# Kernel tuning notes

Measured on AMD Instinct MI355X. Metric: run time of the kernel, lower is better.

Reference implementation:

```python
import jax, jax.numpy as jnp
import numpy as np

N = 100000
E = 1600000
IN_DIM, HID, Z = 128, 64, 32


def gcn_conv(x, src, dst, num_nodes, W, b):
    """PyG GCNConv: add self-loops, symmetric deg^-1/2 normalization.
    x: [N, F_in]; src/dst: [E] int (self-loops already appended by caller wrapper).
    """
    h = x @ W  # [N, F_out] transform first (PyG order)
    ones = jnp.ones(src.shape[0], dtype=x.dtype)
    deg = jax.ops.segment_sum(ones, dst, num_segments=num_nodes)  # in-degree incl. self-loop
    dinv = jnp.where(deg > 0, jax.lax.rsqrt(deg), 0.0)
    norm = dinv[src] * dinv[dst]  # [E]
    msgs = h[src] * norm[:, None]  # [E, F_out] irregular gather
    out = jax.ops.segment_sum(msgs, dst, num_segments=num_nodes)  # scatter-add
    return out + b


def setup_inputs() -> dict:
    key = jax.random.key(0)
    ks = jax.random.split(key, 10)
    x = jax.random.normal(ks[0], (N, IN_DIM), dtype=jnp.float32)
    edge_index = jax.random.randint(ks[1], (2, E), 0, N, dtype=jnp.int64)

    def glorot(k, fan_in, fan_out):
        s = jnp.sqrt(6.0 / (fan_in + fan_out))
        return jax.random.uniform(k, (fan_in, fan_out), jnp.float32, -s, s)

    return {
        "x": x,
        "edge_index": edge_index,
        "W1": glorot(ks[2], IN_DIM, HID),
        "b1": jnp.zeros((HID,), jnp.float32),
        "W2": glorot(ks[3], HID, Z),
        "b2": jnp.zeros((Z,), jnp.float32),
        "Wmu": glorot(ks[4], Z, Z),
        "bmu": jnp.zeros((Z,), jnp.float32),
        "Wlv": glorot(ks[5], Z, Z),
        "blv": jnp.zeros((Z,), jnp.float32),
    }


def reference(x, edge_index, W1, b1, W2, b2, Wmu, bmu, Wlv, blv):
    num_nodes = x.shape[0]
    loop = jnp.arange(num_nodes, dtype=edge_index.dtype)
    src = jnp.concatenate([edge_index[0], loop])  # self-loops appended
    dst = jnp.concatenate([edge_index[1], loop])
    h = jax.nn.relu(gcn_conv(x, src, dst, num_nodes, W1, b1))
    h = gcn_conv(h, src, dst, num_nodes, W2, b2)
    mu = h @ Wmu + bmu
    logvar = h @ Wlv + blv
    return (mu, logvar)
```

## Files before the change

kernel.cpp:

```cpp
#include <hip/hip_runtime.h>

#define N_NODES 100000
#define N_EDGES 1600000
#define IN_F   128
#define HID_F  64
#define Z_F    32
#define NBUK   782
#define BCAP   3072
#define P1T    4096
#define P1_BLOCKS ((N_EDGES + P1T - 1) / P1T)
#define AGG_CAP 2048

typedef unsigned int uint32;
typedef __attribute__((ext_vector_type(8))) short bf16x8;
typedef __attribute__((ext_vector_type(4))) float f32x4;

__device__ __forceinline__ unsigned short f2bf(float f) {
    unsigned u = __float_as_uint(f);
    u = (u + 0x7FFF + ((u >> 16) & 1)) >> 16;
    return (unsigned short)u;
}
__device__ __forceinline__ uint32 pack2bf(float lo, float hi) {
    return (uint32)f2bf(lo) | ((uint32)f2bf(hi) << 16);
}
__device__ __forceinline__ float bflo(uint32 u) { return __uint_as_float(u << 16); }
__device__ __forceinline__ float bfhi(uint32 u) { return __uint_as_float(u & 0xFFFF0000u); }

__global__ __launch_bounds__(256) void phase1_kernel(const int* __restrict__ ei,
                                                     int* __restrict__ gcur,
                                                     uint32* __restrict__ pairs) {
    __shared__ int hist[NBUK];
    __shared__ int lbase[NBUK];
    __shared__ int gbase[NBUK];
    __shared__ int lcur[NBUK];
    __shared__ uint32 stage[P1T];
    __shared__ unsigned short sbid[P1T];
    __shared__ int part[256];
    int tid = threadIdx.x;
    int e0 = blockIdx.x * P1T;
    int ecnt = N_EDGES - e0; if (ecnt > P1T) ecnt = P1T;
    for (int b = tid; b < NBUK; b += 256) { hist[b] = 0; lcur[b] = 0; }
    __syncthreads();
    for (int k = tid; k < ecnt; k += 256)
        atomicAdd(&hist[ei[N_EDGES + e0 + k] >> 7], 1);
    __syncthreads();
    int t4 = tid * 4;
    int l0 = 0, l1 = 0, l2 = 0, l3 = 0, s = 0;
    if (t4 + 0 < NBUK) { l0 = hist[t4 + 0]; s += l0; }
    if (t4 + 1 < NBUK) { l1 = hist[t4 + 1]; s += l1; }
    if (t4 + 2 < NBUK) { l2 = hist[t4 + 2]; s += l2; }
    if (t4 + 3 < NBUK) { l3 = hist[t4 + 3]; s += l3; }
    part[tid] = s;
    __syncthreads();
    for (int off = 1; off < 256; off <<= 1) {
        int add = (tid >= off) ? part[tid - off] : 0;
        __syncthreads();
        part[tid] += add;
        __syncthreads();
    }
    int run = part[tid] - s;
    if (t4 + 0 < NBUK) { lbase[t4 + 0] = run; run += l0; }
    if (t4 + 1 < NBUK) { lbase[t4 + 1] = run; run += l1; }
    if (t4 + 2 < NBUK) { lbase[t4 + 2] = run; run += l2; }
    if (t4 + 3 < NBUK) { lbase[t4 + 3] = run; run += l3; }
    for (int b = tid; b < NBUK; b += 256) {
        int h = hist[b];
        gbase[b] = h ? atomicAdd(&gcur[b], h) : 0;
    }
    __syncthreads();
    for (int k = tid; k < ecnt; k += 256) {
        int sN = ei[e0 + k];
        int d  = ei[N_EDGES + e0 + k];
        int b = d >> 7;
        int slot = lbase[b] + atomicAdd(&lcur[b], 1);
        stage[slot] = (uint32)sN | ((uint32)(d & 127) << 17);
        sbid[slot] = (unsigned short)b;
    }
    __syncthreads();
    for (int k = tid; k < ecnt; k += 256) {
        int b = sbid[k];
        int r = gbase[b] + (k - lbase[b]);
        if (r < BCAP) pairs[(size_t)b * BCAP + r] = stage[k];
    }
}

__global__ void prep_kernel(const int* __restrict__ gcur,
                            const float* __restrict__ W1, const float* __restrict__ W2,
                            const float* __restrict__ Wmu, const float* __restrict__ Wlv,
                            int* __restrict__ bucketBase, int* __restrict__ rowptr,
                            unsigned short* __restrict__ Wt1,
                            unsigned short* __restrict__ Wt2,
                            unsigned short* __restrict__ Wth) {
    __shared__ int s[1024];
    int t = threadIdx.x;
    int v = (t < NBUK) ? gcur[t] : 0;
    s[t] = v;
    __syncthreads();
    for (int off = 1; off < 1024; off <<= 1) {
        int add = (t >= off) ? s[t - off] : 0;
        __syncthreads();
        s[t] += add;
        __syncthreads();
    }
    if (t < NBUK) bucketBase[t] = s[t] - v;
    if (t == 0) rowptr[N_NODES] = N_EDGES;
    for (int i = t; i < IN_F * HID_F; i += 1024) {
        int n = i >> 7, k = i & 127;
        Wt1[i] = f2bf(W1[k * HID_F + n]);
    }
    for (int i = t; i < HID_F * Z_F; i += 1024) {
        int n = i >> 6, k = i & 63;
        Wt2[i] = f2bf(W2[k * Z_F + n]);
    }
    for (int i = t; i < Z_F * 64; i += 1024) {
        int n = i >> 5, k = i & 31;
        Wth[i] = f2bf(n < 32 ? Wmu[k * Z_F + n] : Wlv[k * Z_F + (n - 32)]);
    }
}

__global__ __launch_bounds__(256) void phase2_kernel(const uint32* __restrict__ pairs,
                                                     const int* __restrict__ gcur,
                                                     const int* __restrict__ bucketBase,
                                                     int* __restrict__ rowptr,
                                                     float* __restrict__ dinv,
                                                     int* __restrict__ col) {
    __shared__ int lhist[128];
    __shared__ int lscan[128];
    __shared__ int lcur[128];
    __shared__ int stage[BCAP];
    int b = blockIdx.x;
    int tid = threadIdx.x;
    int cnt_b = gcur[b];
    if (cnt_b > BCAP) cnt_b = BCAP;
    int gbase = bucketBase[b];
    int node0 = b << 7;
    int nb = N_NODES - node0;
    if (nb > 128) nb = 128;
    if (tid < 128) { lhist[tid] = 0; lcur[tid] = 0; }
    __syncthreads();
    const uint32* pb = pairs + (size_t)b * BCAP;
    for (int k = tid; k < cnt_b; k += 256) atomicAdd(&lhist[pb[k] >> 17], 1);
    __syncthreads();
    int v = (tid < 128) ? lhist[tid] : 0;
    if (tid < 128) lscan[tid] = v;
    __syncthreads();
    for (int off = 1; off < 128; off <<= 1) {
        int add = (tid < 128 && tid >= off) ? lscan[tid - off] : 0;
        __syncthreads();
        if (tid < 128) lscan[tid] += add;
        __syncthreads();
    }
    if (tid < 128) lscan[tid] -= v;
    __syncthreads();
    if (tid < nb) {
        rowptr[node0 + tid] = gbase + lscan[tid];
        dinv[node0 + tid] = rsqrtf((float)(lhist[tid] + 1));
    }
    for (int k = tid; k < cnt_b; k += 256) {
        uint32 u = pb[k];
        int ld = u >> 17;
        int r = atomicAdd(&lcur[ld], 1);
        stage[lscan[ld] + r] = (int)(u & 0x1FFFF);
    }
    __syncthreads();
    for (int k = tid; k < cnt_b; k += 256) col[gbase + k] = stage[k];
}

__global__ __launch_bounds__(256) void gemm1_kernel(const float* __restrict__ x,
                                                    const unsigned short* __restrict__ Wt1,
                                                    const float* __restrict__ dinv,
                                                    unsigned short* __restrict__ t1) {
    __shared__ unsigned short Cs[64 * 72];
    __shared__ float dv[64];
    int tid = threadIdx.x;
    int node0 = blockIdx.x * 64;
    if (tid < 64) {
        int n = node0 + tid;
        dv[tid] = (n < N_NODES) ? dinv[n] : 0.f;
    }
    __syncthreads();
    int w = tid >> 6, lane = tid & 63;
    int m = lane & 15, quad = lane >> 4;
    int row = w * 16 + m;
    int node = node0 + row;
    const float* xr = x + (size_t)min(node, N_NODES - 1) * IN_F;
    f32x4 acc0 = {0.f, 0.f, 0.f, 0.f};
    f32x4 acc1 = acc0, acc2 = acc0, acc3 = acc0;
#pragma unroll
    for (int ks = 0; ks < 4; ks++) {
        int kb = ks * 32 + quad * 8;
        float4 f0 = *(const float4*)(xr + kb);
        float4 f1 = *(const float4*)(xr + kb + 4);
        union { bf16x8 v; unsigned short u[8]; } A;
        A.u[0] = f2bf(f0.x); A.u[1] = f2bf(f0.y); A.u[2] = f2bf(f0.z); A.u[3] = f2bf(f0.w);
        A.u[4] = f2bf(f1.x); A.u[5] = f2bf(f1.y); A.u[6] = f2bf(f1.z); A.u[7] = f2bf(f1.w);
        bf16x8 b0 = *(const bf16x8*)&Wt1[(0 * 16 + m) * IN_F + kb];
        bf16x8 b1 = *(const bf16x8*)&Wt1[(1 * 16 + m) * IN_F + kb];
        bf16x8 b2 = *(const bf16x8*)&Wt1[(2 * 16 + m) * IN_F + kb];
        bf16x8 b3 = *(const bf16x8*)&Wt1[(3 * 16 + m) * IN_F + kb];
        acc0 = __builtin_amdgcn_mfma_f32_16x16x32_bf16(A.v, b0, acc0, 0, 0, 0);
        acc1 = __builtin_amdgcn_mfma_f32_16x16x32_bf16(A.v, b1, acc1, 0, 0, 0);
        acc2 = __builtin_amdgcn_mfma_f32_16x16x32_bf16(A.v, b2, acc2, 0, 0, 0);
        acc3 = __builtin_amdgcn_mfma_f32_16x16x32_bf16(A.v, b3, acc3, 0, 0, 0);
    }
    int rbase = w * 16 + quad * 4;
#pragma unroll
    for (int reg = 0; reg < 4; reg++) {
        int r = rbase + reg;
        float d = dv[r];
        Cs[r * 72 +  0 + m] = f2bf(acc0[reg] * d);
        Cs[r * 72 + 16 + m] = f2bf(acc1[reg] * d);
        Cs[r * 72 + 32 + m] = f2bf(acc2[reg] * d);
        Cs[r * 72 + 48 + m] = f2bf(acc3[reg] * d);
    }
    __syncthreads();
#pragma unroll
    for (int it = 0; it < 4; it++) {
        int idx = it * 256 + tid;
        int r = idx >> 4, c = idx & 15;
        int nd = node0 + r;
        if (nd < N_NODES) {
            uint2 vv = *(const uint2*)&Cs[r * 72 + c * 4];
            *(uint2*)&t1[(size_t)nd * HID_F + c * 4] = vv;
        }
    }
}

__global__ __launch_bounds__(256) void agg1gemm2_kernel(const unsigned short* __restrict__ t1,
                                                        const int* __restrict__ rowptr,
                                                        const int* __restrict__ col,
                                                        const float* __restrict__ dinv,
                                                        const float* __restrict__ b1,
                                                        const unsigned short* __restrict__ Wt2,
                                                        unsigned short* __restrict__ t2s) {
    __shared__ int lcol[AGG_CAP];
    __shared__ int lrp[65];
    __shared__ float ldv[64];
    __shared__ unsigned short h1s[64 * 72];
    __shared__ unsigned short Cs[64 * 36];
    int tid = threadIdx.x;
    int node0 = blockIdx.x * 64;
    if (tid < 65) lrp[tid] = rowptr[min(node0 + tid, N_NODES)];
    __syncthreads();
    int s0 = lrp[0];
    int cnt = lrp[64] - s0; if (cnt > AGG_CAP) cnt = AGG_CAP;
    for (int k = tid; k < cnt; k += 256) lcol[k] = col[s0 + k];
    if (tid < 64) {
        int n = node0 + tid;
        ldv[tid] = (n < N_NODES) ? dinv[n] : 0.f;
    }
    __syncthreads();
    int lane = tid & 63, w = tid >> 6;
    int q = lane >> 4, fl = lane & 15;
    int qg = w * 4 + q;
    const uint2* t1v = (const uint2*)t1;
    float4 bb = ((const float4*)b1)[fl];
#pragma unroll
    for (int rep = 0; rep < 4; rep++) {
        int li = qg + rep * 16;
        int node = node0 + li;
        uint2 pk = make_uint2(0u, 0u);
        if (node < N_NODES) {
            int s = lrp[li] - s0;
            int e = lrp[li + 1] - s0; if (e > cnt) e = cnt;
            float a0 = 0.f, a1 = 0.f, a2 = 0.f, a3 = 0.f;
            int p = s;
            for (; p + 3 < e; p += 4) {
                int c0 = lcol[p], c1 = lcol[p + 1], c2 = lcol[p + 2], c3 = lcol[p + 3];
                uint2 u0 = t1v[(size_t)c0 * 16 + fl];
                uint2 u1 = t1v[(size_t)c1 * 16 + fl];
                uint2 u2 = t1v[(size_t)c2 * 16 + fl];
                uint2 u3 = t1v[(size_t)c3 * 16 + fl];
                a0 += bflo(u0.x) + bflo(u1.x) + bflo(u2.x) + bflo(u3.x);
                a1 += bfhi(u0.x) + bfhi(u1.x) + bfhi(u2.x) + bfhi(u3.x);
                a2 += bflo(u0.y) + bflo(u1.y) + bflo(u2.y) + bflo(u3.y);
                a3 += bfhi(u0.y) + bfhi(u1.y) + bfhi(u2.y) + bfhi(u3.y);
            }
            for (; p < e; p++) {
                uint2 u = t1v[(size_t)lcol[p] * 16 + fl];
                a0 += bflo(u.x); a1 += bfhi(u.x);
                a2 += bflo(u.y); a3 += bfhi(u.y);
            }
            uint2 us = t1v[(size_t)node * 16 + fl];
            float di = ldv[li];
            float o0 = fmaxf(di * (a0 + bflo(us.x)) + bb.x, 0.f);
            float o1 = fmaxf(di * (a1 + bfhi(us.x)) + bb.y, 0.f);
            float o2 = fmaxf(di * (a2 + bflo(us.y)) + bb.z, 0.f);
            float o3 = fmaxf(di * (a3 + bfhi(us.y)) + bb.w, 0.f);
            pk.x = pack2bf(o0, o1);
            pk.y = pack2bf(o2, o3);
        }
        *(uint2*)&h1s[li * 72 + fl * 4] = pk;
    }
    __syncthreads();
    int m = lane & 15, quad = lane >> 4;
    int row = w * 16 + m;
    f32x4 acc0 = {0.f, 0.f, 0.f, 0.f};
    f32x4 acc1 = acc0;
#pragma unroll
    for (int ks = 0; ks < 2; ks++) {
        int kb = ks * 32 + quad * 8;
        bf16x8 a  = *(const bf16x8*)&h1s[row * 72 + kb];
        bf16x8 b0 = *(const bf16x8*)&Wt2[(0 * 16 + m) * HID_F + kb];
        bf16x8 b1 = *(const bf16x8*)&Wt2[(1 * 16 + m) * HID_F + kb];
        acc0 = __builtin_amdgcn_mfma_f32_16x16x32_bf16(a, b0, acc0, 0, 0, 0);
        acc1 = __builtin_amdgcn_mfma_f32_16x16x32_bf16(a, b1, acc1, 0, 0, 0);
    }
    int rbase = w * 16 + quad * 4;
#pragma unroll
    for (int reg = 0; reg < 4; reg++) {
        int r = rbase + reg;
        float d = ldv[r];
        Cs[r * 36 +  0 + m] = f2bf(acc0[reg] * d);
        Cs[r * 36 + 16 + m] = f2bf(acc1[reg] * d);
    }
    __syncthreads();
#pragma unroll
    for (int it = 0; it < 2; it++) {
        int idx = it * 256 + tid;
        int r = idx >> 3, c = idx & 7;
        int nd = node0 + r;
        if (nd < N_NODES) {
            uint2 vv = *(const uint2*)&Cs[r * 36 + c * 4];
            *(uint2*)&t2s[(size_t)nd * Z_F + c * 4] = vv;
        }
    }
}

__global__ __launch_bounds__(256) void agg2heads_kernel(const unsigned short* __restrict__ t2s,
                                                        const int* __restrict__ rowptr,
                                                        const int* __restrict__ col,
                                                        const float* __restrict__ dinv,
                                                        const float* __restrict__ b2,
                                                        const unsigned short* __restrict__ Wth,
                                                        const float* __restrict__ bmu,
                                                        const float* __restrict__ blv,
                                                        float* __restrict__ out) {
    __shared__ int lcol[AGG_CAP];
    __shared__ int lrp[65];
    __shared__ float ldv[64];
    __shared__ unsigned short h2s[64 * 40];
    __shared__ float Cf[64 * 68];
    __shared__ float bias[64];
    int tid = threadIdx.x;
    int node0 = blockIdx.x * 64;
    if (tid < 65) lrp[tid] = rowptr[min(node0 + tid, N_NODES)];
    else if (tid >= 96 && tid < 128) bias[tid - 96] = bmu[tid - 96];
    else if (tid >= 128 && tid < 160) bias[tid - 96] = blv[tid - 128];
    __syncthreads();
    int s0 = lrp[0];
    int cnt = lrp[64] - s0; if (cnt > AGG_CAP) cnt = AGG_CAP;
    for (int k = tid; k < cnt; k += 256) lcol[k] = col[s0 + k];
    if (tid < 64) {
        int n = node0 + tid;
        ldv[tid] = (n < N_NODES) ? dinv[n] : 0.f;
    }
    __syncthreads();
    int lane = tid & 63, w = tid >> 6;
    int oc = lane >> 3, fo = lane & 7;
    int og = w * 8 + oc;
    const uint2* t2v = (const uint2*)t2s;
    float4 bb = ((const float4*)b2)[fo];
#pragma unroll
    for (int rep = 0; rep < 2; rep++) {
        int li = og + rep * 32;
        int node = node0 + li;
        uint2 pk = make_uint2(0u, 0u);
        if (node < N_NODES) {
            int s = lrp[li] - s0;
            int e = lrp[li + 1] - s0; if (e > cnt) e = cnt;
            float a0 = 0.f, a1 = 0.f, a2 = 0.f, a3 = 0.f;
            int p = s;
            for (; p + 3 < e; p += 4) {
                int c0 = lcol[p], c1 = lcol[p + 1], c2 = lcol[p + 2], c3 = lcol[p + 3];
                uint2 u0 = t2v[(size_t)c0 * 8 + fo];
                uint2 u1 = t2v[(size_t)c1 * 8 + fo];
                uint2 u2 = t2v[(size_t)c2 * 8 + fo];
                uint2 u3 = t2v[(size_t)c3 * 8 + fo];
                a0 += bflo(u0.x) + bflo(u1.x) + bflo(u2.x) + bflo(u3.x);
                a1 += bfhi(u0.x) + bfhi(u1.x) + bfhi(u2.x) + bfhi(u3.x);
                a2 += bflo(u0.y) + bflo(u1.y) + bflo(u2.y) + bflo(u3.y);
                a3 += bfhi(u0.y) + bfhi(u1.y) + bfhi(u2.y) + bfhi(u3.y);
            }
            for (; p < e; p++) {
                uint2 u = t2v[(size_t)lcol[p] * 8 + fo];
                a0 += bflo(u.x); a1 += bfhi(u.x);
                a2 += bflo(u.y); a3 += bfhi(u.y);
            }
            uint2 us = t2v[(size_t)node * 8 + fo];
            float di = ldv[li];
            float o0 = di * (a0 + bflo(us.x)) + bb.x;
            float o1 = di * (a1 + bfhi(us.x)) + bb.y;
            float o2 = di * (a2 + bflo(us.y)) + bb.z;
            float o3 = di * (a3 + bfhi(us.y)) + bb.w;
            pk.x = pack2bf(o0, o1);
            pk.y = pack2bf(o2, o3);
        }
        *(uint2*)&h2s[li * 40 + fo * 4] = pk;
    }
    __syncthreads();
    int m = lane & 15, quad = lane >> 4;
    int row = w * 16 + m;
    int kb = quad * 8;
    bf16x8 a  = *(const bf16x8*)&h2s[row * 40 + kb];
    bf16x8 b0 = *(const bf16x8*)&Wth[(0 * 16 + m) * Z_F + kb];
    bf16x8 b1 = *(const bf16x8*)&Wth[(1 * 16 + m) * Z_F + kb];
    bf16x8 b2v = *(const bf16x8*)&Wth[(2 * 16 + m) * Z_F + kb];
    bf16x8 b3 = *(const bf16x8*)&Wth[(3 * 16 + m) * Z_F + kb];
    f32x4 acc0 = {0.f, 0.f, 0.f, 0.f};
    f32x4 acc1 = acc0, acc2 = acc0, acc3 = acc0;
    acc0 = __builtin_amdgcn_mfma_f32_16x16x32_bf16(a, b0, acc0, 0, 0, 0);
    acc1 = __builtin_amdgcn_mfma_f32_16x16x32_bf16(a, b1, acc1, 0, 0, 0);
    acc2 = __builtin_amdgcn_mfma_f32_16x16x32_bf16(a, b2v, acc2, 0, 0, 0);
    acc3 = __builtin_amdgcn_mfma_f32_16x16x32_bf16(a, b3, acc3, 0, 0, 0);
    int rbase = w * 16 + quad * 4;
#pragma unroll
    for (int reg = 0; reg < 4; reg++) {
        int r = rbase + reg;
        Cf[r * 68 +  0 + m] = acc0[reg] + bias[ 0 + m];
        Cf[r * 68 + 16 + m] = acc1[reg] + bias[16 + m];
        Cf[r * 68 + 32 + m] = acc2[reg] + bias[32 + m];
        Cf[r * 68 + 48 + m] = acc3[reg] + bias[48 + m];
    }
    __syncthreads();
#pragma unroll
    for (int it = 0; it < 2; it++) {
        int idx = it * 256 + tid;
        int r = idx >> 3, c = idx & 7;
        int nd = node0 + r;
        if (nd < N_NODES) {
            float4 vmu = *(const float4*)&Cf[r * 68 + c * 4];
            float4 vlv = *(const float4*)&Cf[r * 68 + 32 + c * 4];
            *(float4*)&out[(size_t)nd * Z_F + c * 4] = vmu;
            *(float4*)&out[(size_t)N_NODES * Z_F + (size_t)nd * Z_F + c * 4] = vlv;
        }
    }
}

extern "C" void kernel_launch(void* const* d_in, const int* in_sizes, int n_in,
                              void* d_out, int out_size, void* d_ws, size_t ws_size,
                              hipStream_t stream) {
    const float* x   = (const float*)d_in[0];
    const int*   ei  = (const int*)d_in[1];
    const float* W1  = (const float*)d_in[2];
    const float* b1  = (const float*)d_in[3];
    const float* W2  = (const float*)d_in[4];
    const float* b2  = (const float*)d_in[5];
    const float* Wmu = (const float*)d_in[6];
    const float* bmu = (const float*)d_in[7];
    const float* Wlv = (const float*)d_in[8];
    const float* blv = (const float*)d_in[9];
    float* out = (float*)d_out;

    char* ws = (char*)d_ws;
    size_t off = 0;
    auto A = [&](size_t bytes) {
        size_t r = off;
        off += (bytes + 255) & ~(size_t)255;
        return r;
    };
    int*   gcur       = (int*)(ws + A((size_t)NBUK * 4));
    int*   bucketBase = (int*)(ws + A((size_t)NBUK * 4));
    int*   rowptr     = (int*)(ws + A((size_t)(N_NODES + 1) * 4));
    float* dinv       = (float*)(ws + A((size_t)N_NODES * 4));
    unsigned short* Wt1 = (unsigned short*)(ws + A((size_t)IN_F * HID_F * 2));
    unsigned short* Wt2 = (unsigned short*)(ws + A((size_t)HID_F * Z_F * 2));
    unsigned short* Wth = (unsigned short*)(ws + A((size_t)Z_F * 64 * 2));
    int*   col        = (int*)(ws + A((size_t)N_EDGES * 4));
    char*  reg1 = ws + A((size_t)NBUK * BCAP * 4);
    uint32* pairs = (uint32*)reg1;
    unsigned short* t2s = (unsigned short*)reg1;
    unsigned short* t1 = (unsigned short*)(ws + A((size_t)N_NODES * HID_F * 2));

    hipMemsetAsync(gcur, 0, (size_t)NBUK * 4, stream);

    phase1_kernel<<<P1_BLOCKS, 256, 0, stream>>>(ei, gcur, pairs);
    prep_kernel<<<1, 1024, 0, stream>>>(gcur, W1, W2, Wmu, Wlv, bucketBase, rowptr,
                                        Wt1, Wt2, Wth);
    phase2_kernel<<<NBUK, 256, 0, stream>>>(pairs, gcur, bucketBase, rowptr, dinv, col);

    int nblk = (N_NODES + 63) / 64;
    gemm1_kernel<<<nblk, 256, 0, stream>>>(x, Wt1, dinv, t1);
    agg1gemm2_kernel<<<nblk, 256, 0, stream>>>(t1, rowptr, col, dinv, b1, Wt2, t2s);
    agg2heads_kernel<<<nblk, 256, 0, stream>>>(t2s, rowptr, col, dinv, b2, Wth, bmu, blv, out);
}
```

Baseline: 228.6 us.

## Fold prep kernel into phase1/phase2, cache dst in registers, widen aggregation loads

Removes the single-block prep kernel. Weight conversion moves to an extra block of phase1, and each phase2 block now computes its own bucket base by summing gcur with a block reduction. Phase1 keeps the destination indices in registers so it reads them only once. Both aggregation kernels switch from 8-byte to 16-byte gathers with fewer lanes per node. Together these cut one launch, one serialized scan and redundant loads, at the cost of redundant prefix sums in phase2 and more registers.

```diff
diff --git a/kernel.cpp b/kernel.cpp
--- a/kernel.cpp
+++ b/kernel.cpp
@@ -26,9 +26,35 @@
 __device__ __forceinline__ float bflo(uint32 u) { return __uint_as_float(u << 16); }
 __device__ __forceinline__ float bfhi(uint32 u) { return __uint_as_float(u & 0xFFFF0000u); }
 
+#define ACC8(u) { a0 += bflo(u.x); a1 += bfhi(u.x); a2 += bflo(u.y); a3 += bfhi(u.y); \
+                  a4 += bflo(u.z); a5 += bfhi(u.z); a6 += bflo(u.w); a7 += bfhi(u.w); }
+
 __global__ __launch_bounds__(256) void phase1_kernel(const int* __restrict__ ei,
                                                      int* __restrict__ gcur,
-                                                     uint32* __restrict__ pairs) {
+                                                     uint32* __restrict__ pairs,
+                                                     const float* __restrict__ W1,
+                                                     const float* __restrict__ W2,
+                                                     const float* __restrict__ Wmu,
+                                                     const float* __restrict__ Wlv,
+                                                     unsigned short* __restrict__ Wt1,
+                                                     unsigned short* __restrict__ Wt2,
+                                                     unsigned short* __restrict__ Wth) {
+    if (blockIdx.x == P1_BLOCKS) {
+        int t = threadIdx.x;
+        for (int i = t; i < IN_F * HID_F; i += 256) {
+            int n = i >> 7, k = i & 127;
+            Wt1[i] = f2bf(W1[k * HID_F + n]);
+        }
+        for (int i = t; i < HID_F * Z_F; i += 256) {
+            int n = i >> 6, k = i & 63;
+            Wt2[i] = f2bf(W2[k * Z_F + n]);
+        }
+        for (int i = t; i < Z_F * 64; i += 256) {
+            int n = i >> 5, k = i & 31;
+            Wth[i] = f2bf(n < 32 ? Wmu[k * Z_F + n] : Wlv[k * Z_F + (n - 32)]);
+        }
+        return;
+    }
     __shared__ int hist[NBUK];
     __shared__ int lbase[NBUK];
     __shared__ int gbase[NBUK];
@@ -41,8 +67,15 @@
     int ecnt = N_EDGES - e0; if (ecnt > P1T) ecnt = P1T;
     for (int b = tid; b < NBUK; b += 256) { hist[b] = 0; lcur[b] = 0; }
     __syncthreads();
-    for (int k = tid; k < ecnt; k += 256)
-        atomicAdd(&hist[ei[N_EDGES + e0 + k] >> 7], 1);
+    int myd[16];
+#pragma unroll
+    for (int i = 0; i < 16; i++) {
+        int k = tid + i * 256;
+        myd[i] = (k < ecnt) ? ei[N_EDGES + e0 + k] : -1;
+    }
+#pragma unroll
+    for (int i = 0; i < 16; i++)
+        if (myd[i] >= 0) atomicAdd(&hist[myd[i] >> 7], 1);
     __syncthreads();
     int t4 = tid * 4;
     int l0 = 0, l1 = 0, l2 = 0, l3 = 0, s = 0;
@@ -68,13 +101,17 @@
         gbase[b] = h ? atomicAdd(&gcur[b], h) : 0;
     }
     __syncthreads();
-    for (int k = tid; k < ecnt; k += 256) {
-        int sN = ei[e0 + k];
-        int d  = ei[N_EDGES + e0 + k];
-        int b = d >> 7;
-        int slot = lbase[b] + atomicAdd(&lcur[b], 1);
-        stage[slot] = (uint32)sN | ((uint32)(d & 127) << 17);
-        sbid[slot] = (unsigned short)b;
+#pragma unroll
+    for (int i = 0; i < 16; i++) {
+        int k = tid + i * 256;
+        if (k < ecnt) {
+            int sN = ei[e0 + k];
+            int d  = myd[i];
+            int b = d >> 7;
+            int slot = lbase[b] + atomicAdd(&lcur[b], 1);
+            stage[slot] = (uint32)sN | ((uint32)(d & 127) << 17);
+            sbid[slot] = (unsigned short)b;
+        }
     }
     __syncthreads();
     for (int k = tid; k < ecnt; k += 256) {
@@ -84,43 +121,8 @@
     }
 }
 
-__global__ void prep_kernel(const int* __restrict__ gcur,
-                            const float* __restrict__ W1, const float* __restrict__ W2,
-                            const float* __restrict__ Wmu, const float* __restrict__ Wlv,
-                            int* __restrict__ bucketBase, int* __restrict__ rowptr,
-                            unsigned short* __restrict__ Wt1,
-                            unsigned short* __restrict__ Wt2,
-                            unsigned short* __restrict__ Wth) {
-    __shared__ int s[1024];
-    int t = threadIdx.x;
-    int v = (t < NBUK) ? gcur[t] : 0;
-    s[t] = v;
-    __syncthreads();
-    for (int off = 1; off < 1024; off <<= 1) {
-        int add = (t >= off) ? s[t - off] : 0;
-        __syncthreads();
-        s[t] += add;
-        __syncthreads();
-    }
-    if (t < NBUK) bucketBase[t] = s[t] - v;
-    if (t == 0) rowptr[N_NODES] = N_EDGES;
-    for (int i = t; i < IN_F * HID_F; i += 1024) {
-        int n = i >> 7, k = i & 127;
-        Wt1[i] = f2bf(W1[k * HID_F + n]);
-    }
-    for (int i = t; i < HID_F * Z_F; i += 1024) {
-        int n = i >> 6, k = i & 63;
-        Wt2[i] = f2bf(W2[k * Z_F + n]);
-    }
-    for (int i = t; i < Z_F * 64; i += 1024) {
-        int n = i >> 5, k = i & 31;
-        Wth[i] = f2bf(n < 32 ? Wmu[k * Z_F + n] : Wlv[k * Z_F + (n - 32)]);
-    }
-}
-
 __global__ __launch_bounds__(256) void phase2_kernel(const uint32* __restrict__ pairs,
                                                      const int* __restrict__ gcur,
-                                                     const int* __restrict__ bucketBase,
                                                      int* __restrict__ rowptr,
                                                      float* __restrict__ dinv,
                                                      int* __restrict__ col) {
@@ -128,16 +130,22 @@
     __shared__ int lscan[128];
     __shared__ int lcur[128];
     __shared__ int stage[BCAP];
+    __shared__ int wsum[4];
     int b = blockIdx.x;
     int tid = threadIdx.x;
     int cnt_b = gcur[b];
     if (cnt_b > BCAP) cnt_b = BCAP;
-    int gbase = bucketBase[b];
+    int partial = 0;
+    for (int i = tid; i < b; i += 256) partial += gcur[i];
+#pragma unroll
+    for (int off = 32; off > 0; off >>= 1) partial += __shfl_down(partial, off);
+    if (tid < 128) { lhist[tid] = 0; lcur[tid] = 0; }
+    if ((tid & 63) == 0) wsum[tid >> 6] = partial;
+    __syncthreads();
+    int gbase = wsum[0] + wsum[1] + wsum[2] + wsum[3];
     int node0 = b << 7;
     int nb = N_NODES - node0;
     if (nb > 128) nb = 128;
-    if (tid < 128) { lhist[tid] = 0; lcur[tid] = 0; }
-    __syncthreads();
     const uint32* pb = pairs + (size_t)b * BCAP;
     for (int k = tid; k < cnt_b; k += 256) atomicAdd(&lhist[pb[k] >> 17], 1);
     __syncthreads();
@@ -156,6 +164,7 @@
         rowptr[node0 + tid] = gbase + lscan[tid];
         dinv[node0 + tid] = rsqrtf((float)(lhist[tid] + 1));
     }
+    if (b == NBUK - 1 && tid == 0) rowptr[N_NODES] = N_EDGES;
     for (int k = tid; k < cnt_b; k += 256) {
         uint32 u = pb[k];
         int ld = u >> 17;
@@ -251,46 +260,50 @@
     }
     __syncthreads();
     int lane = tid & 63, w = tid >> 6;
-    int q = lane >> 4, fl = lane & 15;
-    int qg = w * 4 + q;
-    const uint2* t1v = (const uint2*)t1;
-    float4 bb = ((const float4*)b1)[fl];
-#pragma unroll
-    for (int rep = 0; rep < 4; rep++) {
-        int li = qg + rep * 16;
+    int grp = lane >> 3, fl = lane & 7;
+    int gg = w * 8 + grp;
+    const uint4* t1q = (const uint4*)t1;
+    float4 bb0 = ((const float4*)b1)[fl * 2];
+    float4 bb1 = ((const float4*)b1)[fl * 2 + 1];
+#pragma unroll
+    for (int rep = 0; rep < 2; rep++) {
+        int li = gg + rep * 32;
         int node = node0 + li;
-        uint2 pk = make_uint2(0u, 0u);
+        uint4 pk = make_uint4(0u, 0u, 0u, 0u);
         if (node < N_NODES) {
             int s = lrp[li] - s0;
             int e = lrp[li + 1] - s0; if (e > cnt) e = cnt;
             float a0 = 0.f, a1 = 0.f, a2 = 0.f, a3 = 0.f;
+            float a4 = 0.f, a5 = 0.f, a6 = 0.f, a7 = 0.f;
             int p = s;
             for (; p + 3 < e; p += 4) {
                 int c0 = lcol[p], c1 = lcol[p + 1], c2 = lcol[p + 2], c3 = lcol[p + 3];
-                uint2 u0 = t1v[(size_t)c0 * 16 + fl];
-                uint2 u1 = t1v[(size_t)c1 * 16 + fl];
-                uint2 u2 = t1v[(size_t)c2 * 16 + fl];
-                uint2 u3 = t1v[(size_t)c3 * 16 + fl];
-                a0 += bflo(u0.x) + bflo(u1.x) + bflo(u2.x) + bflo(u3.x);
-                a1 += bfhi(u0.x) + bfhi(u1.x) + bfhi(u2.x) + bfhi(u3.x);
-                a2 += bflo(u0.y) + bflo(u1.y) + bflo(u2.y) + bflo(u3.y);
-                a3 += bfhi(u0.y) + bfhi(u1.y) + bfhi(u2.y) + bfhi(u3.y);
+                uint4 u0 = t1q[(size_t)c0 * 8 + fl];
+                uint4 u1 = t1q[(size_t)c1 * 8 + fl];
+                uint4 u2 = t1q[(size_t)c2 * 8 + fl];
+                uint4 u3 = t1q[(size_t)c3 * 8 + fl];
+                ACC8(u0); ACC8(u1); ACC8(u2); ACC8(u3);
             }
             for (; p < e; p++) {
-                uint2 u = t1v[(size_t)lcol[p] * 16 + fl];
-                a0 += bflo(u.x); a1 += bfhi(u.x);
-                a2 += bflo(u.y); a3 += bfhi(u.y);
+                uint4 u = t1q[(size_t)lcol[p] * 8 + fl];
+                ACC8(u);
             }
-            uint2 us = t1v[(size_t)node * 16 + fl];
+            uint4 us = t1q[(size_t)node * 8 + fl];
             float di = ldv[li];
-            float o0 = fmaxf(di * (a0 + bflo(us.x)) + bb.x, 0.f);
-            float o1 = fmaxf(di * (a1 + bfhi(us.x)) + bb.y, 0.f);
-            float o2 = fmaxf(di * (a2 + bflo(us.y)) + bb.z, 0.f);
-            float o3 = fmaxf(di * (a3 + bfhi(us.y)) + bb.w, 0.f);
+            float o0 = fmaxf(di * (a0 + bflo(us.x)) + bb0.x, 0.f);
+            float o1 = fmaxf(di * (a1 + bfhi(us.x)) + bb0.y, 0.f);
+            float o2 = fmaxf(di * (a2 + bflo(us.y)) + bb0.z, 0.f);
+            float o3 = fmaxf(di * (a3 + bfhi(us.y)) + bb0.w, 0.f);
+            float o4 = fmaxf(di * (a4 + bflo(us.z)) + bb1.x, 0.f);
+            float o5 = fmaxf(di * (a5 + bfhi(us.z)) + bb1.y, 0.f);
+            float o6 = fmaxf(di * (a6 + bflo(us.w)) + bb1.z, 0.f);
+            float o7 = fmaxf(di * (a7 + bfhi(us.w)) + bb1.w, 0.f);
             pk.x = pack2bf(o0, o1);
             pk.y = pack2bf(o2, o3);
-        }
-        *(uint2*)&h1s[li * 72 + fl * 4] = pk;
+            pk.z = pack2bf(o4, o5);
+            pk.w = pack2bf(o6, o7);
+        }
+        *(uint4*)&h1s[li * 72 + fl * 8] = pk;
     }
     __syncthreads();
     int m = lane & 15, quad = lane >> 4;
@@ -302,9 +315,9 @@
         int kb = ks * 32 + quad * 8;
         bf16x8 a  = *(const bf16x8*)&h1s[row * 72 + kb];
         bf16x8 b0 = *(const bf16x8*)&Wt2[(0 * 16 + m) * HID_F + kb];
-        bf16x8 b1 = *(const bf16x8*)&Wt2[(1 * 16 + m) * HID_F + kb];
+        bf16x8 b1v = *(const bf16x8*)&Wt2[(1 * 16 + m) * HID_F + kb];
         acc0 = __builtin_amdgcn_mfma_f32_16x16x32_bf16(a, b0, acc0, 0, 0, 0);
-        acc1 = __builtin_amdgcn_mfma_f32_16x16x32_bf16(a, b1, acc1, 0, 0, 0);
+        acc1 = __builtin_amdgcn_mfma_f32_16x16x32_bf16(a, b1v, acc1, 0, 0, 0);
     }
     int rbase = w * 16 + quad * 4;
 #pragma unroll
@@ -357,46 +370,48 @@
     }
     __syncthreads();
     int lane = tid & 63, w = tid >> 6;
-    int oc = lane >> 3, fo = lane & 7;
-    int og = w * 8 + oc;
-    const uint2* t2v = (const uint2*)t2s;
-    float4 bb = ((const float4*)b2)[fo];
-#pragma unroll
-    for (int rep = 0; rep < 2; rep++) {
-        int li = og + rep * 32;
+    int grp = lane >> 2, fo = lane & 3;
+    int li = w * 16 + grp;
+    const uint4* t2q = (const uint4*)t2s;
+    float4 bb0 = ((const float4*)b2)[fo * 2];
+    float4 bb1 = ((const float4*)b2)[fo * 2 + 1];
+    {
         int node = node0 + li;
-        uint2 pk = make_uint2(0u, 0u);
+        uint4 pk = make_uint4(0u, 0u, 0u, 0u);
         if (node < N_NODES) {
             int s = lrp[li] - s0;
             int e = lrp[li + 1] - s0; if (e > cnt) e = cnt;
             float a0 = 0.f, a1 = 0.f, a2 = 0.f, a3 = 0.f;
+            float a4 = 0.f, a5 = 0.f, a6 = 0.f, a7 = 0.f;
             int p = s;
             for (; p + 3 < e; p += 4) {
                 int c0 = lcol[p], c1 = lcol[p + 1], c2 = lcol[p + 2], c3 = lcol[p + 3];
-                uint2 u0 = t2v[(size_t)c0 * 8 + fo];
-                uint2 u1 = t2v[(size_t)c1 * 8 + fo];
-                uint2 u2 = t2v[(size_t)c2 * 8 + fo];
-                uint2 u3 = t2v[(size_t)c3 * 8 + fo];
-                a0 += bflo(u0.x) + bflo(u1.x) + bflo(u2.x) + bflo(u3.x);
-                a1 += bfhi(u0.x) + bfhi(u1.x) + bfhi(u2.x) + bfhi(u3.x);
-                a2 += bflo(u0.y) + bflo(u1.y) + bflo(u2.y) + bflo(u3.y);
-                a3 += bfhi(u0.y) + bfhi(u1.y) + bfhi(u2.y) + bfhi(u3.y);
+                uint4 u0 = t2q[(size_t)c0 * 4 + fo];
+                uint4 u1 = t2q[(size_t)c1 * 4 + fo];
+                uint4 u2 = t2q[(size_t)c2 * 4 + fo];
+                uint4 u3 = t2q[(size_t)c3 * 4 + fo];
+                ACC8(u0); ACC8(u1); ACC8(u2); ACC8(u3);
             }
             for (; p < e; p++) {
-                uint2 u = t2v[(size_t)lcol[p] * 8 + fo];
-                a0 += bflo(u.x); a1 += bfhi(u.x);
-                a2 += bflo(u.y); a3 += bfhi(u.y);
+                uint4 u = t2q[(size_t)lcol[p] * 4 + fo];
+                ACC8(u);
             }
-            uint2 us = t2v[(size_t)node * 8 + fo];
+            uint4 us = t2q[(size_t)node * 4 + fo];
             float di = ldv[li];
-            float o0 = di * (a0 + bflo(us.x)) + bb.x;
-            float o1 = di * (a1 + bfhi(us.x)) + bb.y;
-            float o2 = di * (a2 + bflo(us.y)) + bb.z;
-            float o3 = di * (a3 + bfhi(us.y)) + bb.w;
+            float o0 = di * (a0 + bflo(us.x)) + bb0.x;
+            float o1 = di * (a1 + bfhi(us.x)) + bb0.y;
+            float o2 = di * (a2 + bflo(us.y)) + bb0.z;
+            float o3 = di * (a3 + bfhi(us.y)) + bb0.w;
+            float o4 = di * (a4 + bflo(us.z)) + bb1.x;
+            float o5 = di * (a5 + bfhi(us.z)) + bb1.y;
+            float o6 = di * (a6 + bflo(us.w)) + bb1.z;
+            float o7 = di * (a7 + bfhi(us.w)) + bb1.w;
             pk.x = pack2bf(o0, o1);
             pk.y = pack2bf(o2, o3);
-        }
-        *(uint2*)&h2s[li * 40 + fo * 4] = pk;
+            pk.z = pack2bf(o4, o5);
+            pk.w = pack2bf(o6, o7);
+        }
+        *(uint4*)&h2s[li * 40 + fo * 8] = pk;
     }
     __syncthreads();
     int m = lane & 15, quad = lane >> 4;
@@ -460,7 +475,6 @@
         return r;
     };
     int*   gcur       = (int*)(ws + A((size_t)NBUK * 4));
-    int*   bucketBase = (int*)(ws + A((size_t)NBUK * 4));
     int*   rowptr     = (int*)(ws + A((size_t)(N_NODES + 1) * 4));
     float* dinv       = (float*)(ws + A((size_t)N_NODES * 4));
     unsigned short* Wt1 = (unsigned short*)(ws + A((size_t)IN_F * HID_F * 2));
@@ -474,10 +488,9 @@
 
     hipMemsetAsync(gcur, 0, (size_t)NBUK * 4, stream);
 
-    phase1_kernel<<<P1_BLOCKS, 256, 0, stream>>>(ei, gcur, pairs);
-    prep_kernel<<<1, 1024, 0, stream>>>(gcur, W1, W2, Wmu, Wlv, bucketBase, rowptr,
-                                        Wt1, Wt2, Wth);
-    phase2_kernel<<<NBUK, 256, 0, stream>>>(pairs, gcur, bucketBase, rowptr, dinv, col);
+    phase1_kernel<<<P1_BLOCKS + 1, 256, 0, stream>>>(ei, gcur, pairs,
+                                                     W1, W2, Wmu, Wlv, Wt1, Wt2, Wth);
+    phase2_kernel<<<NBUK, 256, 0, stream>>>(pairs, gcur, rowptr, dinv, col);
 
     int nblk = (N_NODES + 63) / 64;
     gemm1_kernel<<<nblk, 256, 0, stream>>>(x, Wt1, dinv, t1);
```

After: 213.5 us. -6.6%, faster.
